# Performance work log

Hardware: AMD Instinct MI355X
Metric: run time of the kernel (lower is better)

Reference implementation:

```python
import jax, jax.numpy as jnp
import numpy as np

B, S, D, H, DK, FF, NQ = 4, 1024, 512, 64, 8, 2048, 8


def _layernorm(x, w, b, eps=1e-5):
    m = x.mean(-1, keepdims=True)
    v = ((x - m) ** 2).mean(-1, keepdims=True)
    return (x - m) / jnp.sqrt(v + eps) * w + b


def setup_inputs() -> dict:
    key = jax.random.key(0)
    ks = jax.random.split(key, 24)
    std = 0.02
    inp = {
        "x": jax.random.normal(ks[0], (B, S, D), dtype=jnp.float32),
        "Wq": jax.random.normal(ks[1], (D, D)) * std,
        "bq": jnp.zeros((D,)),
        "Wk": jax.random.normal(ks[2], (D, D)) * std,
        "bk": jnp.zeros((D,)),
        "Wv": jax.random.normal(ks[3], (D, D)) * std,
        "bv": jnp.zeros((D,)),
        "theta_attn": jax.random.normal(ks[4], (DK,)) * 0.1,  # trainable RX angles
        "gate_attn": jnp.asarray(1.0, dtype=jnp.float32),
        "Wo": jax.random.normal(ks[5], (D, D)) * std,
        "bo": jnp.zeros((D,)),
        "ln1_w": jnp.ones((D,)),
        "ln1_b": jnp.zeros((D,)),
        "W1": jax.random.normal(ks[6], (FF, NQ)) * std,
        "b1": jnp.zeros((FF,)),
        "W2": jax.random.normal(ks[7], (D, FF)) * std,
        "b2": jnp.zeros((D,)),
        "phi_ffn": jax.random.normal(ks[8], (NQ,)) * 0.1,  # trainable RY angles
        "gate_ffn": jnp.asarray(1.0, dtype=jnp.float32),
        "ln2_w": jnp.ones((D,)),
        "ln2_b": jnp.zeros((D,)),
    }
    return inp


def _attention(x, Wq, bq, Wk, bk, Wv, bv, theta, gate, Wo, bo):
    q = x @ Wq.T + bq
    k = x @ Wk.T + bk
    v = x @ Wv.T + bv
    sep = lambda t: t.reshape(B, S, H, DK).transpose(0, 2, 1, 3)  # [B,H,S,DK]
    qh, kh, vh = sep(q), sep(k), sep(v)
    scores = jnp.einsum("bhsd,bhtd->bhst", qh, kh) / np.sqrt(DK)
    probs = jax.nn.softmax(scores, axis=-1)
    classical = jnp.einsum("bhst,bhtd->bhsd", probs, vh)
    classical = classical.transpose(0, 2, 1, 3).reshape(B, S, D)
    # Quantum head: RX(x_i) then RX(theta_i) -> RX(x_i+theta_i), CNOT ring, <Z_j>.
    # Analytic expectations: <Z_0> = prod_{k=1..DK-1} cos(a_k);
    #                        <Z_j> = prod_{k=0..j}    cos(a_k)   (j >= 1).
    cos_a = jnp.cos(qh + theta)  # [B,H,S,DK]
    cp = jnp.cumprod(cos_a, axis=-1)
    z0 = jnp.prod(cos_a[..., 1:], axis=-1, keepdims=True)
    quantum = jnp.concatenate([z0, cp[..., 1:]], axis=-1)  # [B,H,S,DK]
    quantum = quantum.transpose(0, 2, 1, 3).reshape(B, S, D)
    out = gate * quantum + (1.0 - gate) * classical
    return out @ Wo.T + bo


def _ffn(x, W1, b1, W2, b2, phi, gate):
    xs = x[..., :NQ]  # encoder uses first NQ features
    # Quantum: RX(x_i) then RY(phi_i), measure <Z_i> = cos(x_i)*cos(phi_i).
    qm = jnp.cos(xs) * jnp.cos(phi)
    quantum = jax.nn.relu(qm @ W1.T + b1) @ W2.T + b2
    classical = jax.nn.relu(xs @ W1.T + b1) @ W2.T + b2
    return gate * quantum + (1.0 - gate) * classical


def reference(x, Wq, bq, Wk, bk, Wv, bv, theta_attn, gate_attn, Wo, bo,
              ln1_w, ln1_b, W1, b1, W2, b2, phi_ffn, gate_ffn, ln2_w, ln2_b):
    attn_out = _attention(x, Wq, bq, Wk, bk, Wv, bv, theta_attn, gate_attn, Wo, bo)
    x1 = _layernorm(x + attn_out, ln1_w, ln1_b)
    ffn_out = _ffn(x1, W1, b1, W2, b2, phi_ffn, gate_ffn)
    return _layernorm(x1 + ffn_out, ln2_w, ln2_b)
```

## Files before the change

### kernel.cpp

```cpp
#include <hip/hip_runtime.h>
#include <hip/hip_bf16.h>


typedef short short8 __attribute__((ext_vector_type(8)));
typedef float floatx4 __attribute__((ext_vector_type(4)));

__device__ __forceinline__ unsigned short f2bf_bits(float f) {
  __hip_bfloat16 h = __float2bfloat16(f);
  return *reinterpret_cast<unsigned short*>(&h);
}

#define GLOBAL_LOAD_LDS16(g, l)                                               \
  __builtin_amdgcn_global_load_lds(                                           \
      (const __attribute__((address_space(1))) void*)(g),                     \
      (__attribute__((address_space(3))) void*)(l), 16, 0, 0)

#define WAIT_VMCNT0()   asm volatile("s_waitcnt vmcnt(0)" ::: "memory")
#define WAIT_VMCNT16()  asm volatile("s_waitcnt vmcnt(16)" ::: "memory")
#define WAIT_LGKM0()    asm volatile("s_waitcnt lgkmcnt(0)" ::: "memory")

__global__ __launch_bounds__(64) void gemm64(
    const __hip_bfloat16* __restrict__ A,
    const __hip_bfloat16* __restrict__ W,
    const __hip_bfloat16* __restrict__ Wb,
    const float* __restrict__ bias,
    const float* __restrict__ biasb,
    float* __restrict__ Cf,
    float* __restrict__ Cfb,
    __hip_bfloat16* __restrict__ Cb,
    int M, int N, int K, int mode,
    const float* __restrict__ theta,
    const float* __restrict__ gate,
    __hip_bfloat16* __restrict__ mixout,
    const float* __restrict__ skipgate)
{
  if (skipgate != nullptr && *skipgate == 1.0f) return;
  if (blockIdx.z == 1) { W = Wb; bias = biasb; Cf = Cfb; }
  __shared__ __align__(16) __hip_bfloat16 sh[16384];
  const int lane = threadIdx.x;
  const long m0 = (long)blockIdx.x * 64;
  const long n0 = (long)blockIdx.y * 64;

  floatx4 acc[4][4];
#pragma unroll
  for (int i = 0; i < 4; ++i)
#pragma unroll
    for (int j = 0; j < 4; ++j)
      acc[i][j] = (floatx4){0.f, 0.f, 0.f, 0.f};

  const int srow = lane >> 3;
  const int schunk = lane & 7;
  const int gchunk = schunk ^ srow;
  const int frow = lane & 15;
  const int fk = lane >> 4;

  auto stage = [&](int kt, __hip_bfloat16* Ab, __hip_bfloat16* Bb) {
#pragma unroll
    for (int ib = 0; ib < 8; ++ib) {
      const int row = ib * 8 + srow;
      GLOBAL_LOAD_LDS16(A + (m0 + row) * K + kt + gchunk * 8, Ab + ib * 512);
      GLOBAL_LOAD_LDS16(W + (n0 + row) * K + kt + gchunk * 8, Bb + ib * 512);
    }
  };

  const int ntiles = K >> 6;
  stage(0, sh, sh + 4096);
  for (int t = 0; t < ntiles; ++t) {
    __hip_bfloat16* As = sh + (t & 1) * 8192;
    __hip_bfloat16* Bs = As + 4096;
    if (t + 1 < ntiles) {
      WAIT_LGKM0();
      __hip_bfloat16* An = sh + ((t + 1) & 1) * 8192;
      stage((t + 1) << 6, An, An + 4096);
      WAIT_VMCNT16();
    } else {
      WAIT_VMCNT0();
    }
    short8 af[2][4], bf[2][4];
#pragma unroll
    for (int ks = 0; ks < 2; ++ks)
#pragma unroll
      for (int i = 0; i < 4; ++i) {
        const int ar = i * 16 + frow;
        af[ks][i] = *(const short8*)(As + ar * 64 + (((ks * 4 + fk) ^ (ar & 7)) << 3));
        bf[ks][i] = *(const short8*)(Bs + ar * 64 + (((ks * 4 + fk) ^ (ar & 7)) << 3));
      }
#pragma unroll
    for (int ks = 0; ks < 2; ++ks)
#pragma unroll
      for (int i = 0; i < 4; ++i)
#pragma unroll
        for (int j = 0; j < 4; ++j)
          acc[i][j] = __builtin_amdgcn_mfma_f32_16x16x32_bf16(
              af[ks][i], bf[ks][j], acc[i][j], 0, 0, 0);
  }

  const int col_l = lane & 15;
  const int row_l = (lane >> 4) << 2;

  if (mode == 0 || (mode == 1 && *gate != 1.0f)) {
#pragma unroll
    for (int j = 0; j < 4; ++j) {
      const long col = n0 + j * 16 + col_l;
      const float bv = bias ? bias[col] : 0.0f;
#pragma unroll
      for (int i = 0; i < 4; ++i)
#pragma unroll
        for (int r = 0; r < 4; ++r)
          Cf[(m0 + i * 16 + row_l + r) * N + col] = acc[i][j][r] + bv;
    }
  }
  if (mode == 2) {
#pragma unroll
    for (int j = 0; j < 4; ++j) {
      const long col = n0 + j * 16 + col_l;
      const float bv = bias ? bias[col] : 0.0f;
#pragma unroll
      for (int i = 0; i < 4; ++i)
#pragma unroll
        for (int r = 0; r < 4; ++r)
          Cb[(m0 + i * 16 + row_l + r) * N + col] =
              __float2bfloat16(fmaxf(acc[i][j][r] + bv, 0.0f));
    }
  }
  if (mode == 1) {
    float* shf = (float*)sh;
    WAIT_LGKM0();
#pragma unroll
    for (int j = 0; j < 4; ++j) {
      const long col = n0 + j * 16 + col_l;
      const float bv = bias ? bias[col] : 0.0f;
#pragma unroll
      for (int i = 0; i < 4; ++i)
#pragma unroll
        for (int r = 0; r < 4; ++r)
          shf[(i * 16 + row_l + r) * 64 + j * 16 + col_l] = acc[i][j][r] + bv;
    }
    WAIT_LGKM0();
    float th[8];
#pragma unroll
    for (int i = 0; i < 8; ++i) th[i] = theta[i];
#pragma unroll
    for (int t = 0; t < 8; ++t) {
      const int gidx = t * 64 + lane;
      const int row = gidx >> 3;
      const int hh = gidx & 7;
      const float* src = shf + row * 64 + hh * 8;
      float c[8];
#pragma unroll
      for (int i = 0; i < 8; ++i) c[i] = __cosf(src[i] + th[i]);
      float o[8];
      float p = c[1];
#pragma unroll
      for (int i = 2; i < 8; ++i) p *= c[i];
      o[0] = p;
      float cp = c[0];
#pragma unroll
      for (int i = 1; i < 8; ++i) { cp *= c[i]; o[i] = cp; }
      union { unsigned short u16[8]; uint4 v; } pk;
#pragma unroll
      for (int i = 0; i < 8; ++i) pk.u16[i] = f2bf_bits(o[i]);
      *(uint4*)(mixout + (m0 + row) * N + n0 + hh * 8) = pk.v;
    }
  }
}

__device__ __forceinline__ void cvt_one(const float* s, __hip_bfloat16* d, int n,
                                        long tid, long stride) {
  const int n4 = n >> 2;
  for (long i = tid; i < n4; i += stride) {
    float4 v = ((const float4*)s)[i];
    ushort4 u;
    u.x = f2bf_bits(v.x); u.y = f2bf_bits(v.y);
    u.z = f2bf_bits(v.z); u.w = f2bf_bits(v.w);
    ((ushort4*)d)[i] = u;
  }
}

__global__ __launch_bounds__(256) void prep_inputs(
    const float* x, __hip_bfloat16* x_bf,
    const float* Wq, __hip_bfloat16* Wq_bf,
    const float* Wo, __hip_bfloat16* Wo_bf,
    const float* W2, __hip_bfloat16* W2_bf,
    const float* W1, __hip_bfloat16* W1_pad,
    const float* Wk, __hip_bfloat16* Wk_bf,
    const float* Wv, __hip_bfloat16* Wv_bf,
    const float* gateA)
{
  const long stride = (long)gridDim.x * blockDim.x;
  const long tid = (long)blockIdx.x * blockDim.x + threadIdx.x;
  cvt_one(x, x_bf, 4096 * 512, tid, stride);
  cvt_one(Wq, Wq_bf, 512 * 512, tid, stride);
  cvt_one(Wo, Wo_bf, 512 * 512, tid, stride);
  cvt_one(W2, W2_bf, 512 * 2048, tid, stride);
  for (long g = tid; g < 2048 * 16; g += stride) {
    const int row = g >> 4;
    const int c4 = (g & 15) << 2;
    ushort4 u = {0, 0, 0, 0};
    if (c4 < 8) {
      float4 v = *(const float4*)(W1 + row * 8 + c4);
      u.x = f2bf_bits(v.x); u.y = f2bf_bits(v.y);
      u.z = f2bf_bits(v.z); u.w = f2bf_bits(v.w);
    }
    ((ushort4*)W1_pad)[g] = u;
  }
  if (*gateA != 1.0f) {
    cvt_one(Wk, Wk_bf, 512 * 512, tid, stride);
    cvt_one(Wv, Wv_bf, 512 * 512, tid, stride);
  }
}

__global__ __launch_bounds__(256) void lnffn(
    const float* __restrict__ x, const float* __restrict__ attn,
    const float* __restrict__ w, const float* __restrict__ bias,
    float* __restrict__ x1, const float* __restrict__ phi,
    __hip_bfloat16* __restrict__ qm_pad, __hip_bfloat16* __restrict__ xs_pad,
    const float* __restrict__ gateF)
{
  const int row = blockIdx.x;
  const int tid = threadIdx.x;
  const long base = (long)row * 512;
  const int c0 = tid * 2;
  float2 av = *(const float2*)(x + base + c0);
  float2 bv = *(const float2*)(attn + base + c0);
  float s0 = av.x + bv.x, s1 = av.y + bv.y;
  float sum = s0 + s1, ssq = s0 * s0 + s1 * s1;
#pragma unroll
  for (int off = 32; off > 0; off >>= 1) {
    sum += __shfl_down(sum, off);
    ssq += __shfl_down(ssq, off);
  }
  __shared__ float red[8];
  __shared__ float qtmp[8];
  const int wv = tid >> 6, ln = tid & 63;
  if (ln == 0) { red[wv] = sum; red[4 + wv] = ssq; }
  __syncthreads();
  if (tid == 0) {
    float ts = red[0] + red[1] + red[2] + red[3];
    float tq = red[4] + red[5] + red[6] + red[7];
    float mean = ts * (1.0f / 512.0f);
    float var = tq * (1.0f / 512.0f) - mean * mean;
    red[0] = mean;
    red[1] = rsqrtf(fmaxf(var, 0.0f) + 1e-5f);
  }
  __syncthreads();
  const float mean = red[0], rstd = red[1];
  const float o0 = (s0 - mean) * rstd * w[c0] + bias[c0];
  const float o1 = (s1 - mean) * rstd * w[c0 + 1] + bias[c0 + 1];
  float2 ov; ov.x = o0; ov.y = o1;
  *(float2*)(x1 + base + c0) = ov;
  if (c0 < 8) { qtmp[c0] = o0; qtmp[c0 + 1] = o1; }
  __syncthreads();
  const float gf = *gateF;
  if (tid < 32) {
    ushort2 q = {0, 0};
    if (c0 < 8) {
      q.x = f2bf_bits(__cosf(qtmp[c0]) * __cosf(phi[c0]));
      q.y = f2bf_bits(__cosf(qtmp[c0 + 1]) * __cosf(phi[c0 + 1]));
    }
    *(ushort2*)(qm_pad + (long)row * 64 + c0) = q;
    if (gf != 1.0f) {
      ushort2 xs = {0, 0};
      if (c0 < 8) { xs.x = f2bf_bits(qtmp[c0]); xs.y = f2bf_bits(qtmp[c0 + 1]); }
      *(ushort2*)(xs_pad + (long)row * 64 + c0) = xs;
    }
  }
}

__global__ __launch_bounds__(256) void add_ln2(
    const float* __restrict__ a, const float* __restrict__ b,
    const float* __restrict__ b_alt, const float* __restrict__ gate,
    const float* __restrict__ w, const float* __restrict__ bias,
    float* __restrict__ out)
{
  const int row = blockIdx.x;
  const int tid = threadIdx.x;
  const long base = (long)row * 512;
  const int c0 = tid * 2;
  float2 av = *(const float2*)(a + base + c0);
  float2 bv = *(const float2*)(b + base + c0);
  float s0, s1;
  const float gv = *gate;
  if (gv != 1.0f) {
    float2 cv = *(const float2*)(b_alt + base + c0);
    s0 = av.x + gv * bv.x + (1.0f - gv) * cv.x;
    s1 = av.y + gv * bv.y + (1.0f - gv) * cv.y;
  } else {
    s0 = av.x + bv.x;
    s1 = av.y + bv.y;
  }
  float sum = s0 + s1, ssq = s0 * s0 + s1 * s1;
#pragma unroll
  for (int off = 32; off > 0; off >>= 1) {
    sum += __shfl_down(sum, off);
    ssq += __shfl_down(ssq, off);
  }
  __shared__ float red[8];
  const int wv = tid >> 6, ln = tid & 63;
  if (ln == 0) { red[wv] = sum; red[4 + wv] = ssq; }
  __syncthreads();
  if (tid == 0) {
    float ts = red[0] + red[1] + red[2] + red[3];
    float tq = red[4] + red[5] + red[6] + red[7];
    float mean = ts * (1.0f / 512.0f);
    float var = tq * (1.0f / 512.0f) - mean * mean;
    red[0] = mean;
    red[1] = rsqrtf(fmaxf(var, 0.0f) + 1e-5f);
  }
  __syncthreads();
  const float mean = red[0], rstd = red[1];
  float2 ov;
  ov.x = (s0 - mean) * rstd * w[c0] + bias[c0];
  ov.y = (s1 - mean) * rstd * w[c0 + 1] + bias[c0 + 1];
  *(float2*)(out + base + c0) = ov;
}

__global__ __launch_bounds__(256) void mixfix(
    __hip_bfloat16* __restrict__ mix, const float* __restrict__ cls,
    const float* __restrict__ gate, int n)
{
  const float g = *gate;
  if (g == 1.0f) return;
  const long stride = (long)gridDim.x * blockDim.x;
  for (long i = (long)blockIdx.x * blockDim.x + threadIdx.x; i < n; i += stride) {
    float q = __bfloat162float(mix[i]);
    mix[i] = __float2bfloat16(g * q + (1.0f - g) * cls[i]);
  }
}

__global__ __launch_bounds__(256) void attn_classical(
    const float* __restrict__ Q, const float* __restrict__ Kb,
    const float* __restrict__ Vb, float* __restrict__ cls,
    const float* __restrict__ skipgate)
{
  if (*skipgate == 1.0f) return;
  const int idx = blockIdx.x * blockDim.x + threadIdx.x;
  if (idx >= 4 * 64 * 1024) return;
  const int s = idx & 1023;
  const int h = (idx >> 10) & 63;
  const int b = idx >> 16;
  const long qoff = ((long)(b * 1024 + s)) * 512 + h * 8;
  float q[8];
#pragma unroll
  for (int i = 0; i < 8; ++i) q[i] = Q[qoff + i] * 0.35355339059327373f;
  float m = -INFINITY, l = 0.0f, acc[8];
#pragma unroll
  for (int i = 0; i < 8; ++i) acc[i] = 0.0f;
  for (int t = 0; t < 1024; ++t) {
    const long koff = ((long)(b * 1024 + t)) * 512 + h * 8;
    const float* kr = Kb + koff;
    const float* vr = Vb + koff;
    float sc = 0.0f;
#pragma unroll
    for (int i = 0; i < 8; ++i) sc += q[i] * kr[i];
    float nm = fmaxf(m, sc);
    float corr = __expf(m - nm);
    float p = __expf(sc - nm);
    l = l * corr + p;
#pragma unroll
    for (int i = 0; i < 8; ++i) acc[i] = acc[i] * corr + p * vr[i];
    m = nm;
  }
  const float inv = 1.0f / l;
#pragma unroll
  for (int i = 0; i < 8; ++i) cls[qoff + i] = acc[i] * inv;
}

extern "C" void kernel_launch(void* const* d_in, const int* in_sizes, int n_in,
                              void* d_out, int out_size, void* d_ws, size_t ws_size,
                              hipStream_t stream) {
  const float* x     = (const float*)d_in[0];
  const float* Wq    = (const float*)d_in[1];
  const float* bq    = (const float*)d_in[2];
  const float* Wk    = (const float*)d_in[3];
  const float* bk    = (const float*)d_in[4];
  const float* Wv    = (const float*)d_in[5];
  const float* bv    = (const float*)d_in[6];
  const float* theta = (const float*)d_in[7];
  const float* gateA = (const float*)d_in[8];
  const float* Wo    = (const float*)d_in[9];
  const float* bo    = (const float*)d_in[10];
  const float* ln1w  = (const float*)d_in[11];
  const float* ln1b  = (const float*)d_in[12];
  const float* W1    = (const float*)d_in[13];
  const float* b1    = (const float*)d_in[14];
  const float* W2    = (const float*)d_in[15];
  const float* b2    = (const float*)d_in[16];
  const float* phi   = (const float*)d_in[17];
  const float* gateF = (const float*)d_in[18];
  const float* ln2w  = (const float*)d_in[19];
  const float* ln2b  = (const float*)d_in[20];
  float* out = (float*)d_out;

  const size_t MB = 1024 * 1024;
  char* wsb = (char*)d_ws;
  __hip_bfloat16* x_bf   = (__hip_bfloat16*)(wsb + 0 * MB);
  __hip_bfloat16* Wq_bf  = (__hip_bfloat16*)(wsb + 4 * MB);
  __hip_bfloat16* Wo_bf  = (__hip_bfloat16*)(wsb + 4 * MB + 512 * 1024);
  __hip_bfloat16* W2_bf  = (__hip_bfloat16*)(wsb + 5 * MB);
  __hip_bfloat16* W1_pad = (__hip_bfloat16*)(wsb + 7 * MB);
  __hip_bfloat16* qm_pad = (__hip_bfloat16*)(wsb + 7 * MB + 512 * 1024);
  __hip_bfloat16* mix_bf = (__hip_bfloat16*)(wsb + 8 * MB);
  float*          attn   = (float*)(wsb + 12 * MB);
  float*          x1     = (float*)(wsb + 20 * MB);
  __hip_bfloat16* hq_bf  = (__hip_bfloat16*)(wsb + 28 * MB);
  float*          Fb     = (float*)(wsb + 44 * MB);
  float*          Qb     = (float*)(wsb + 52 * MB);
  __hip_bfloat16* Wk_bf  = (__hip_bfloat16*)(wsb + 60 * MB);
  __hip_bfloat16* Wv_bf  = (__hip_bfloat16*)(wsb + 60 * MB + 512 * 1024);
  float*          Kb2    = (float*)(wsb + 61 * MB);
  float*          Vb2    = (float*)(wsb + 69 * MB);
  float*          clsb   = (float*)(wsb + 77 * MB);
  __hip_bfloat16* xs_pad = (__hip_bfloat16*)(wsb + 85 * MB);
  __hip_bfloat16* hc_bf  = (__hip_bfloat16*)(wsb + 86 * MB);
  float*          Fc     = (float*)(wsb + 102 * MB);

  prep_inputs<<<1024, 256, 0, stream>>>(
      x, x_bf, Wq, Wq_bf, Wo, Wo_bf, W2, W2_bf, W1, W1_pad,
      Wk, Wk_bf, Wv, Wv_bf, gateA);
  gemm64<<<dim3(64, 8), 64, 0, stream>>>(
      x_bf, Wq_bf, nullptr, bq, nullptr, Qb, nullptr, nullptr,
      4096, 512, 512, 1, theta, gateA, mix_bf, nullptr);
  gemm64<<<dim3(64, 8, 2), 64, 0, stream>>>(
      x_bf, Wk_bf, Wv_bf, bk, bv, Kb2, Vb2, nullptr,
      4096, 512, 512, 0, nullptr, nullptr, nullptr, gateA);
  attn_classical<<<1024, 256, 0, stream>>>(Qb, Kb2, Vb2, clsb, gateA);
  mixfix<<<512, 256, 0, stream>>>(mix_bf, clsb, gateA, 4096 * 512);
  gemm64<<<dim3(64, 8), 64, 0, stream>>>(
      mix_bf, Wo_bf, nullptr, bo, nullptr, attn, nullptr, nullptr,
      4096, 512, 512, 0, nullptr, nullptr, nullptr, nullptr);
  lnffn<<<4096, 256, 0, stream>>>(x, attn, ln1w, ln1b, x1, phi,
                                  qm_pad, xs_pad, gateF);
  gemm64<<<dim3(64, 32), 64, 0, stream>>>(
      qm_pad, W1_pad, nullptr, b1, nullptr, nullptr, nullptr, hq_bf,
      4096, 2048, 64, 2, nullptr, nullptr, nullptr, nullptr);
  gemm64<<<dim3(64, 32), 64, 0, stream>>>(
      xs_pad, W1_pad, nullptr, b1, nullptr, nullptr, nullptr, hc_bf,
      4096, 2048, 64, 2, nullptr, nullptr, nullptr, gateF);
  gemm64<<<dim3(64, 8), 64, 0, stream>>>(
      hq_bf, W2_bf, nullptr, b2, nullptr, Fb, nullptr, nullptr,
      4096, 512, 2048, 0, nullptr, nullptr, nullptr, nullptr);
  gemm64<<<dim3(64, 8), 64, 0, stream>>>(
      hc_bf, W2_bf, nullptr, b2, nullptr, Fc, nullptr, nullptr,
      4096, 512, 2048, 0, nullptr, nullptr, nullptr, gateF);
  add_ln2<<<4096, 256, 0, stream>>>(x1, Fb, Fc, gateF, ln2w, ln2b, out);
}
```

Measured before the change: 175.2 us.

## Fuse W1 projection into LayerNorm kernel and merge QKV/FFN-out launches

Replaces the K=64 padded MFMA GEMM for the 8-wide W1 projection with direct FMA inside a new LayerNorm kernel that writes the ReLU hidden activations. The QKV and two FFN-output GEMMs each become a single launch that picks its operand by blockIdx.z, and the classical attention now blends straight into the mix buffer, removing the separate mixfix pass. LayerNorm kernels are rewritten to one wave per row with vectorized loads, dropping block-level syncs. This cuts launch count and the padded-GEMM and intermediate-buffer traffic, in exchange for a heavier per-thread inner product in lnffn2.

```diff
diff --git a/kernel.cpp b/kernel.cpp
--- a/kernel.cpp
+++ b/kernel.cpp
@@ -8,6 +8,11 @@
 __device__ __forceinline__ unsigned short f2bf_bits(float f) {
   __hip_bfloat16 h = __float2bfloat16(f);
   return *reinterpret_cast<unsigned short*>(&h);
+}
+__device__ __forceinline__ float bfbits2f(unsigned short u) {
+  union { unsigned int u; float f; } c;
+  c.u = (unsigned int)u << 16;
+  return c.f;
 }
 
 #define GLOBAL_LOAD_LDS16(g, l)                                               \
@@ -19,35 +24,12 @@
 #define WAIT_VMCNT16()  asm volatile("s_waitcnt vmcnt(16)" ::: "memory")
 #define WAIT_LGKM0()    asm volatile("s_waitcnt lgkmcnt(0)" ::: "memory")
 
-__global__ __launch_bounds__(64) void gemm64(
+__device__ __forceinline__ void gemm_core(
     const __hip_bfloat16* __restrict__ A,
     const __hip_bfloat16* __restrict__ W,
-    const __hip_bfloat16* __restrict__ Wb,
-    const float* __restrict__ bias,
-    const float* __restrict__ biasb,
-    float* __restrict__ Cf,
-    float* __restrict__ Cfb,
-    __hip_bfloat16* __restrict__ Cb,
-    int M, int N, int K, int mode,
-    const float* __restrict__ theta,
-    const float* __restrict__ gate,
-    __hip_bfloat16* __restrict__ mixout,
-    const float* __restrict__ skipgate)
-{
-  if (skipgate != nullptr && *skipgate == 1.0f) return;
-  if (blockIdx.z == 1) { W = Wb; bias = biasb; Cf = Cfb; }
-  __shared__ __align__(16) __hip_bfloat16 sh[16384];
-  const int lane = threadIdx.x;
-  const long m0 = (long)blockIdx.x * 64;
-  const long n0 = (long)blockIdx.y * 64;
-
-  floatx4 acc[4][4];
-#pragma unroll
-  for (int i = 0; i < 4; ++i)
-#pragma unroll
-    for (int j = 0; j < 4; ++j)
-      acc[i][j] = (floatx4){0.f, 0.f, 0.f, 0.f};
-
+    int K, long m0, long n0, int lane,
+    __hip_bfloat16* sh, floatx4 acc[4][4])
+{
   const int srow = lane >> 3;
   const int schunk = lane & 7;
   const int gchunk = schunk ^ srow;
@@ -94,42 +76,60 @@
           acc[i][j] = __builtin_amdgcn_mfma_f32_16x16x32_bf16(
               af[ks][i], bf[ks][j], acc[i][j], 0, 0, 0);
   }
+}
+
+__global__ __launch_bounds__(64) void gemm_qkv(
+    const __hip_bfloat16* __restrict__ x_bf,
+    const __hip_bfloat16* __restrict__ Wq,
+    const __hip_bfloat16* __restrict__ Wk,
+    const __hip_bfloat16* __restrict__ Wv,
+    const float* __restrict__ bq, const float* __restrict__ bk,
+    const float* __restrict__ bvv,
+    __hip_bfloat16* __restrict__ mix,
+    float* __restrict__ Qb, float* __restrict__ Kb, float* __restrict__ Vb,
+    const float* __restrict__ theta, const float* __restrict__ gateA)
+{
+  const int z = blockIdx.z;
+  const float g = *gateA;
+  if (z > 0 && g == 1.0f) return;
+  const __hip_bfloat16* W = (z == 0) ? Wq : (z == 1) ? Wk : Wv;
+  const float* bias = (z == 0) ? bq : (z == 1) ? bk : bvv;
+  float* Cf = (z == 0) ? Qb : (z == 1) ? Kb : Vb;
+
+  __shared__ __align__(16) __hip_bfloat16 sh[16384];
+  const int lane = threadIdx.x;
+  const long m0 = (long)blockIdx.x * 64;
+  const long n0 = (long)blockIdx.y * 64;
+  floatx4 acc[4][4];
+#pragma unroll
+  for (int i = 0; i < 4; ++i)
+#pragma unroll
+    for (int j = 0; j < 4; ++j) acc[i][j] = (floatx4){0.f, 0.f, 0.f, 0.f};
+
+  gemm_core(x_bf, W, 512, m0, n0, lane, sh, acc);
 
   const int col_l = lane & 15;
   const int row_l = (lane >> 4) << 2;
 
-  if (mode == 0 || (mode == 1 && *gate != 1.0f)) {
+  if (z > 0 || g != 1.0f) {
 #pragma unroll
     for (int j = 0; j < 4; ++j) {
       const long col = n0 + j * 16 + col_l;
-      const float bv = bias ? bias[col] : 0.0f;
+      const float bv = bias[col];
 #pragma unroll
       for (int i = 0; i < 4; ++i)
 #pragma unroll
         for (int r = 0; r < 4; ++r)
-          Cf[(m0 + i * 16 + row_l + r) * N + col] = acc[i][j][r] + bv;
-    }
-  }
-  if (mode == 2) {
+          Cf[(m0 + i * 16 + row_l + r) * 512 + col] = acc[i][j][r] + bv;
+    }
+  }
+  if (z == 0) {
+    float* shf = (float*)sh;
+    WAIT_LGKM0();
 #pragma unroll
     for (int j = 0; j < 4; ++j) {
       const long col = n0 + j * 16 + col_l;
-      const float bv = bias ? bias[col] : 0.0f;
-#pragma unroll
-      for (int i = 0; i < 4; ++i)
-#pragma unroll
-        for (int r = 0; r < 4; ++r)
-          Cb[(m0 + i * 16 + row_l + r) * N + col] =
-              __float2bfloat16(fmaxf(acc[i][j][r] + bv, 0.0f));
-    }
-  }
-  if (mode == 1) {
-    float* shf = (float*)sh;
-    WAIT_LGKM0();
-#pragma unroll
-    for (int j = 0; j < 4; ++j) {
-      const long col = n0 + j * 16 + col_l;
-      const float bv = bias ? bias[col] : 0.0f;
+      const float bv = bias[col];
 #pragma unroll
       for (int i = 0; i < 4; ++i)
 #pragma unroll
@@ -160,8 +160,72 @@
       union { unsigned short u16[8]; uint4 v; } pk;
 #pragma unroll
       for (int i = 0; i < 8; ++i) pk.u16[i] = f2bf_bits(o[i]);
-      *(uint4*)(mixout + (m0 + row) * N + n0 + hh * 8) = pk.v;
-    }
+      *(uint4*)(mix + (m0 + row) * 512 + n0 + hh * 8) = pk.v;
+    }
+  }
+}
+
+__global__ __launch_bounds__(64) void gemm_plain(
+    const __hip_bfloat16* __restrict__ A,
+    const __hip_bfloat16* __restrict__ W,
+    const float* __restrict__ bias, float* __restrict__ C, int N, int K)
+{
+  __shared__ __align__(16) __hip_bfloat16 sh[16384];
+  const int lane = threadIdx.x;
+  const long m0 = (long)blockIdx.x * 64;
+  const long n0 = (long)blockIdx.y * 64;
+  floatx4 acc[4][4];
+#pragma unroll
+  for (int i = 0; i < 4; ++i)
+#pragma unroll
+    for (int j = 0; j < 4; ++j) acc[i][j] = (floatx4){0.f, 0.f, 0.f, 0.f};
+  gemm_core(A, W, K, m0, n0, lane, sh, acc);
+  const int col_l = lane & 15;
+  const int row_l = (lane >> 4) << 2;
+#pragma unroll
+  for (int j = 0; j < 4; ++j) {
+    const long col = n0 + j * 16 + col_l;
+    const float bv = bias[col];
+#pragma unroll
+    for (int i = 0; i < 4; ++i)
+#pragma unroll
+      for (int r = 0; r < 4; ++r)
+        C[(m0 + i * 16 + row_l + r) * N + col] = acc[i][j][r] + bv;
+  }
+}
+
+__global__ __launch_bounds__(64) void gemm_ffnout(
+    const __hip_bfloat16* __restrict__ hq,
+    const __hip_bfloat16* __restrict__ hc,
+    const __hip_bfloat16* __restrict__ W2, const float* __restrict__ b2,
+    float* __restrict__ Fb, float* __restrict__ Fc,
+    const float* __restrict__ gateF)
+{
+  const int z = blockIdx.z;
+  if (z == 1 && *gateF == 1.0f) return;
+  const __hip_bfloat16* A = z ? hc : hq;
+  float* C = z ? Fc : Fb;
+  __shared__ __align__(16) __hip_bfloat16 sh[16384];
+  const int lane = threadIdx.x;
+  const long m0 = (long)blockIdx.x * 64;
+  const long n0 = (long)blockIdx.y * 64;
+  floatx4 acc[4][4];
+#pragma unroll
+  for (int i = 0; i < 4; ++i)
+#pragma unroll
+    for (int j = 0; j < 4; ++j) acc[i][j] = (floatx4){0.f, 0.f, 0.f, 0.f};
+  gemm_core(A, W2, 2048, m0, n0, lane, sh, acc);
+  const int col_l = lane & 15;
+  const int row_l = (lane >> 4) << 2;
+#pragma unroll
+  for (int j = 0; j < 4; ++j) {
+    const long col = n0 + j * 16 + col_l;
+    const float bv = b2[col];
+#pragma unroll
+    for (int i = 0; i < 4; ++i)
+#pragma unroll
+      for (int r = 0; r < 4; ++r)
+        C[(m0 + i * 16 + row_l + r) * 512 + col] = acc[i][j][r] + bv;
   }
 }
 
@@ -182,7 +246,7 @@
     const float* Wq, __hip_bfloat16* Wq_bf,
     const float* Wo, __hip_bfloat16* Wo_bf,
     const float* W2, __hip_bfloat16* W2_bf,
-    const float* W1, __hip_bfloat16* W1_pad,
+    const float* W1, __hip_bfloat16* W1_bf,
     const float* Wk, __hip_bfloat16* Wk_bf,
     const float* Wv, __hip_bfloat16* Wv_bf,
     const float* gateA)
@@ -193,147 +257,20 @@
   cvt_one(Wq, Wq_bf, 512 * 512, tid, stride);
   cvt_one(Wo, Wo_bf, 512 * 512, tid, stride);
   cvt_one(W2, W2_bf, 512 * 2048, tid, stride);
-  for (long g = tid; g < 2048 * 16; g += stride) {
-    const int row = g >> 4;
-    const int c4 = (g & 15) << 2;
-    ushort4 u = {0, 0, 0, 0};
-    if (c4 < 8) {
-      float4 v = *(const float4*)(W1 + row * 8 + c4);
-      u.x = f2bf_bits(v.x); u.y = f2bf_bits(v.y);
-      u.z = f2bf_bits(v.z); u.w = f2bf_bits(v.w);
-    }
-    ((ushort4*)W1_pad)[g] = u;
-  }
+  cvt_one(W1, W1_bf, 2048 * 8, tid, stride);
   if (*gateA != 1.0f) {
     cvt_one(Wk, Wk_bf, 512 * 512, tid, stride);
     cvt_one(Wv, Wv_bf, 512 * 512, tid, stride);
   }
 }
 
-__global__ __launch_bounds__(256) void lnffn(
-    const float* __restrict__ x, const float* __restrict__ attn,
-    const float* __restrict__ w, const float* __restrict__ bias,
-    float* __restrict__ x1, const float* __restrict__ phi,
-    __hip_bfloat16* __restrict__ qm_pad, __hip_bfloat16* __restrict__ xs_pad,
-    const float* __restrict__ gateF)
-{
-  const int row = blockIdx.x;
-  const int tid = threadIdx.x;
-  const long base = (long)row * 512;
-  const int c0 = tid * 2;
-  float2 av = *(const float2*)(x + base + c0);
-  float2 bv = *(const float2*)(attn + base + c0);
-  float s0 = av.x + bv.x, s1 = av.y + bv.y;
-  float sum = s0 + s1, ssq = s0 * s0 + s1 * s1;
-#pragma unroll
-  for (int off = 32; off > 0; off >>= 1) {
-    sum += __shfl_down(sum, off);
-    ssq += __shfl_down(ssq, off);
-  }
-  __shared__ float red[8];
-  __shared__ float qtmp[8];
-  const int wv = tid >> 6, ln = tid & 63;
-  if (ln == 0) { red[wv] = sum; red[4 + wv] = ssq; }
-  __syncthreads();
-  if (tid == 0) {
-    float ts = red[0] + red[1] + red[2] + red[3];
-    float tq = red[4] + red[5] + red[6] + red[7];
-    float mean = ts * (1.0f / 512.0f);
-    float var = tq * (1.0f / 512.0f) - mean * mean;
-    red[0] = mean;
-    red[1] = rsqrtf(fmaxf(var, 0.0f) + 1e-5f);
-  }
-  __syncthreads();
-  const float mean = red[0], rstd = red[1];
-  const float o0 = (s0 - mean) * rstd * w[c0] + bias[c0];
-  const float o1 = (s1 - mean) * rstd * w[c0 + 1] + bias[c0 + 1];
-  float2 ov; ov.x = o0; ov.y = o1;
-  *(float2*)(x1 + base + c0) = ov;
-  if (c0 < 8) { qtmp[c0] = o0; qtmp[c0 + 1] = o1; }
-  __syncthreads();
-  const float gf = *gateF;
-  if (tid < 32) {
-    ushort2 q = {0, 0};
-    if (c0 < 8) {
-      q.x = f2bf_bits(__cosf(qtmp[c0]) * __cosf(phi[c0]));
-      q.y = f2bf_bits(__cosf(qtmp[c0 + 1]) * __cosf(phi[c0 + 1]));
-    }
-    *(ushort2*)(qm_pad + (long)row * 64 + c0) = q;
-    if (gf != 1.0f) {
-      ushort2 xs = {0, 0};
-      if (c0 < 8) { xs.x = f2bf_bits(qtmp[c0]); xs.y = f2bf_bits(qtmp[c0 + 1]); }
-      *(ushort2*)(xs_pad + (long)row * 64 + c0) = xs;
-    }
-  }
-}
-
-__global__ __launch_bounds__(256) void add_ln2(
-    const float* __restrict__ a, const float* __restrict__ b,
-    const float* __restrict__ b_alt, const float* __restrict__ gate,
-    const float* __restrict__ w, const float* __restrict__ bias,
-    float* __restrict__ out)
-{
-  const int row = blockIdx.x;
-  const int tid = threadIdx.x;
-  const long base = (long)row * 512;
-  const int c0 = tid * 2;
-  float2 av = *(const float2*)(a + base + c0);
-  float2 bv = *(const float2*)(b + base + c0);
-  float s0, s1;
-  const float gv = *gate;
-  if (gv != 1.0f) {
-    float2 cv = *(const float2*)(b_alt + base + c0);
-    s0 = av.x + gv * bv.x + (1.0f - gv) * cv.x;
-    s1 = av.y + gv * bv.y + (1.0f - gv) * cv.y;
-  } else {
-    s0 = av.x + bv.x;
-    s1 = av.y + bv.y;
-  }
-  float sum = s0 + s1, ssq = s0 * s0 + s1 * s1;
-#pragma unroll
-  for (int off = 32; off > 0; off >>= 1) {
-    sum += __shfl_down(sum, off);
-    ssq += __shfl_down(ssq, off);
-  }
-  __shared__ float red[8];
-  const int wv = tid >> 6, ln = tid & 63;
-  if (ln == 0) { red[wv] = sum; red[4 + wv] = ssq; }
-  __syncthreads();
-  if (tid == 0) {
-    float ts = red[0] + red[1] + red[2] + red[3];
-    float tq = red[4] + red[5] + red[6] + red[7];
-    float mean = ts * (1.0f / 512.0f);
-    float var = tq * (1.0f / 512.0f) - mean * mean;
-    red[0] = mean;
-    red[1] = rsqrtf(fmaxf(var, 0.0f) + 1e-5f);
-  }
-  __syncthreads();
-  const float mean = red[0], rstd = red[1];
-  float2 ov;
-  ov.x = (s0 - mean) * rstd * w[c0] + bias[c0];
-  ov.y = (s1 - mean) * rstd * w[c0 + 1] + bias[c0 + 1];
-  *(float2*)(out + base + c0) = ov;
-}
-
-__global__ __launch_bounds__(256) void mixfix(
-    __hip_bfloat16* __restrict__ mix, const float* __restrict__ cls,
-    const float* __restrict__ gate, int n)
-{
-  const float g = *gate;
+__global__ __launch_bounds__(256) void attn_blend(
+    const float* __restrict__ Qb, const float* __restrict__ Kb,
+    const float* __restrict__ Vb, __hip_bfloat16* __restrict__ mix,
+    const float* __restrict__ gateA)
+{
+  const float g = *gateA;
   if (g == 1.0f) return;
-  const long stride = (long)gridDim.x * blockDim.x;
-  for (long i = (long)blockIdx.x * blockDim.x + threadIdx.x; i < n; i += stride) {
-    float q = __bfloat162float(mix[i]);
-    mix[i] = __float2bfloat16(g * q + (1.0f - g) * cls[i]);
-  }
-}
-
-__global__ __launch_bounds__(256) void attn_classical(
-    const float* __restrict__ Q, const float* __restrict__ Kb,
-    const float* __restrict__ Vb, float* __restrict__ cls,
-    const float* __restrict__ skipgate)
-{
-  if (*skipgate == 1.0f) return;
   const int idx = blockIdx.x * blockDim.x + threadIdx.x;
   if (idx >= 4 * 64 * 1024) return;
   const int s = idx & 1023;
@@ -342,7 +279,7 @@
   const long qoff = ((long)(b * 1024 + s)) * 512 + h * 8;
   float q[8];
 #pragma unroll
-  for (int i = 0; i < 8; ++i) q[i] = Q[qoff + i] * 0.35355339059327373f;
+  for (int i = 0; i < 8; ++i) q[i] = Qb[qoff + i] * 0.35355339059327373f;
   float m = -INFINITY, l = 0.0f, acc[8];
 #pragma unroll
   for (int i = 0; i < 8; ++i) acc[i] = 0.0f;
@@ -362,8 +299,163 @@
     m = nm;
   }
   const float inv = 1.0f / l;
-#pragma unroll
-  for (int i = 0; i < 8; ++i) cls[qoff + i] = acc[i] * inv;
+  union { unsigned short u16[8]; uint4 v; } pk;
+  pk.v = *(const uint4*)(mix + qoff);
+#pragma unroll
+  for (int i = 0; i < 8; ++i) {
+    float quant = bfbits2f(pk.u16[i]);
+    pk.u16[i] = f2bf_bits(g * quant + (1.0f - g) * acc[i] * inv);
+  }
+  *(uint4*)(mix + qoff) = pk.v;
+}
+
+__global__ __launch_bounds__(256) void lnffn2(
+    const float* __restrict__ x, const float* __restrict__ attn,
+    const float* __restrict__ lw, const float* __restrict__ lb,
+    float* __restrict__ x1, const float* __restrict__ phi,
+    const __hip_bfloat16* __restrict__ W1_bf, const float* __restrict__ b1,
+    __hip_bfloat16* __restrict__ hq, __hip_bfloat16* __restrict__ hc,
+    const float* __restrict__ gateF)
+{
+  const int tid = threadIdx.x;
+  const int wv = tid >> 6, lane = tid & 63;
+  const int row = blockIdx.x * 4 + wv;
+  const long base = (long)row * 512;
+  const int c0 = lane * 8;
+  __shared__ float qrow[4][8];
+  __shared__ float xsrow[4][8];
+
+  float4 a0 = *(const float4*)(x + base + c0);
+  float4 a1 = *(const float4*)(x + base + c0 + 4);
+  float4 b0 = *(const float4*)(attn + base + c0);
+  float4 b1v4 = *(const float4*)(attn + base + c0 + 4);
+  float s[8] = {a0.x + b0.x, a0.y + b0.y, a0.z + b0.z, a0.w + b0.w,
+                a1.x + b1v4.x, a1.y + b1v4.y, a1.z + b1v4.z, a1.w + b1v4.w};
+  float sum = 0.f, ssq = 0.f;
+#pragma unroll
+  for (int i = 0; i < 8; ++i) { sum += s[i]; ssq += s[i] * s[i]; }
+#pragma unroll
+  for (int off = 32; off > 0; off >>= 1) {
+    sum += __shfl_xor(sum, off);
+    ssq += __shfl_xor(ssq, off);
+  }
+  const float mean = sum * (1.0f / 512.0f);
+  const float var = ssq * (1.0f / 512.0f) - mean * mean;
+  const float rstd = rsqrtf(fmaxf(var, 0.0f) + 1e-5f);
+  float4 w0 = *(const float4*)(lw + c0);
+  float4 w1 = *(const float4*)(lw + c0 + 4);
+  float4 g0 = *(const float4*)(lb + c0);
+  float4 g1 = *(const float4*)(lb + c0 + 4);
+  float o[8];
+  const float wf[8] = {w0.x, w0.y, w0.z, w0.w, w1.x, w1.y, w1.z, w1.w};
+  const float gf8[8] = {g0.x, g0.y, g0.z, g0.w, g1.x, g1.y, g1.z, g1.w};
+#pragma unroll
+  for (int i = 0; i < 8; ++i) o[i] = (s[i] - mean) * rstd * wf[i] + gf8[i];
+  *(float4*)(x1 + base + c0) = (float4){o[0], o[1], o[2], o[3]};
+  *(float4*)(x1 + base + c0 + 4) = (float4){o[4], o[5], o[6], o[7]};
+  if (lane == 0) {
+#pragma unroll
+    for (int i = 0; i < 8; ++i) {
+      qrow[wv][i] = __cosf(o[i]) * __cosf(phi[i]);
+      xsrow[wv][i] = o[i];
+    }
+  }
+  __syncthreads();
+
+  float w1f[8][8];
+#pragma unroll
+  for (int j = 0; j < 8; ++j) {
+    uint4 wr = *(const uint4*)(W1_bf + (long)(tid * 8 + j) * 8);
+    const unsigned short* pu = (const unsigned short*)&wr;
+#pragma unroll
+    for (int k = 0; k < 8; ++k) w1f[j][k] = bfbits2f(pu[k]);
+  }
+  float4 bb0 = *(const float4*)(b1 + tid * 8);
+  float4 bb1 = *(const float4*)(b1 + tid * 8 + 4);
+  const float b1v[8] = {bb0.x, bb0.y, bb0.z, bb0.w, bb1.x, bb1.y, bb1.z, bb1.w};
+  const float gv = *gateF;
+#pragma unroll
+  for (int r = 0; r < 4; ++r) {
+    const long rowr = (long)blockIdx.x * 4 + r;
+    float qm[8];
+#pragma unroll
+    for (int k = 0; k < 8; ++k) qm[k] = qrow[r][k];
+    union { unsigned short u16[8]; uint4 v; } pk;
+#pragma unroll
+    for (int j = 0; j < 8; ++j) {
+      float acc = b1v[j];
+#pragma unroll
+      for (int k = 0; k < 8; ++k) acc += qm[k] * w1f[j][k];
+      pk.u16[j] = f2bf_bits(fmaxf(acc, 0.0f));
+    }
+    *(uint4*)(hq + rowr * 2048 + tid * 8) = pk.v;
+    if (gv != 1.0f) {
+      float xs[8];
+#pragma unroll
+      for (int k = 0; k < 8; ++k) xs[k] = xsrow[r][k];
+#pragma unroll
+      for (int j = 0; j < 8; ++j) {
+        float acc = b1v[j];
+#pragma unroll
+        for (int k = 0; k < 8; ++k) acc += xs[k] * w1f[j][k];
+        pk.u16[j] = f2bf_bits(fmaxf(acc, 0.0f));
+      }
+      *(uint4*)(hc + rowr * 2048 + tid * 8) = pk.v;
+    }
+  }
+}
+
+__global__ __launch_bounds__(256) void add_ln3(
+    const float* __restrict__ x1, const float* __restrict__ Fb,
+    const float* __restrict__ Fc, const float* __restrict__ gateF,
+    const float* __restrict__ lw, const float* __restrict__ lb,
+    float* __restrict__ out)
+{
+  const int tid = threadIdx.x;
+  const int wv = tid >> 6, lane = tid & 63;
+  const int row = blockIdx.x * 4 + wv;
+  const long base = (long)row * 512;
+  const int c0 = lane * 8;
+  float4 a0 = *(const float4*)(x1 + base + c0);
+  float4 a1 = *(const float4*)(x1 + base + c0 + 4);
+  float4 f0 = *(const float4*)(Fb + base + c0);
+  float4 f1 = *(const float4*)(Fb + base + c0 + 4);
+  float s[8];
+  const float gv = *gateF;
+  if (gv != 1.0f) {
+    float4 c0v = *(const float4*)(Fc + base + c0);
+    float4 c1v = *(const float4*)(Fc + base + c0 + 4);
+    const float om = 1.0f - gv;
+    s[0] = a0.x + gv * f0.x + om * c0v.x; s[1] = a0.y + gv * f0.y + om * c0v.y;
+    s[2] = a0.z + gv * f0.z + om * c0v.z; s[3] = a0.w + gv * f0.w + om * c0v.w;
+    s[4] = a1.x + gv * f1.x + om * c1v.x; s[5] = a1.y + gv * f1.y + om * c1v.y;
+    s[6] = a1.z + gv * f1.z + om * c1v.z; s[7] = a1.w + gv * f1.w + om * c1v.w;
+  } else {
+    s[0] = a0.x + f0.x; s[1] = a0.y + f0.y; s[2] = a0.z + f0.z; s[3] = a0.w + f0.w;
+    s[4] = a1.x + f1.x; s[5] = a1.y + f1.y; s[6] = a1.z + f1.z; s[7] = a1.w + f1.w;
+  }
+  float sum = 0.f, ssq = 0.f;
+#pragma unroll
+  for (int i = 0; i < 8; ++i) { sum += s[i]; ssq += s[i] * s[i]; }
+#pragma unroll
+  for (int off = 32; off > 0; off >>= 1) {
+    sum += __shfl_xor(sum, off);
+    ssq += __shfl_xor(ssq, off);
+  }
+  const float mean = sum * (1.0f / 512.0f);
+  const float var = ssq * (1.0f / 512.0f) - mean * mean;
+  const float rstd = rsqrtf(fmaxf(var, 0.0f) + 1e-5f);
+  float4 w0 = *(const float4*)(lw + c0);
+  float4 w1 = *(const float4*)(lw + c0 + 4);
+  float4 g0 = *(const float4*)(lb + c0);
+  float4 g1 = *(const float4*)(lb + c0 + 4);
+  const float wf[8] = {w0.x, w0.y, w0.z, w0.w, w1.x, w1.y, w1.z, w1.w};
+  const float gf8[8] = {g0.x, g0.y, g0.z, g0.w, g1.x, g1.y, g1.z, g1.w};
+  float o[8];
+#pragma unroll
+  for (int i = 0; i < 8; ++i) o[i] = (s[i] - mean) * rstd * wf[i] + gf8[i];
+  *(float4*)(out + base + c0) = (float4){o[0], o[1], o[2], o[3]};
+  *(float4*)(out + base + c0 + 4) = (float4){o[4], o[5], o[6], o[7]};
 }
 
 extern "C" void kernel_launch(void* const* d_in, const int* in_sizes, int n_in,
@@ -398,8 +490,7 @@
   __hip_bfloat16* Wq_bf  = (__hip_bfloat16*)(wsb + 4 * MB);
   __hip_bfloat16* Wo_bf  = (__hip_bfloat16*)(wsb + 4 * MB + 512 * 1024);
   __hip_bfloat16* W2_bf  = (__hip_bfloat16*)(wsb + 5 * MB);
-  __hip_bfloat16* W1_pad = (__hip_bfloat16*)(wsb + 7 * MB);
-  __hip_bfloat16* qm_pad = (__hip_bfloat16*)(wsb + 7 * MB + 512 * 1024);
+  __hip_bfloat16* W1_bf  = (__hip_bfloat16*)(wsb + 7 * MB);
   __hip_bfloat16* mix_bf = (__hip_bfloat16*)(wsb + 8 * MB);
   float*          attn   = (float*)(wsb + 12 * MB);
   float*          x1     = (float*)(wsb + 20 * MB);
@@ -410,38 +501,21 @@
   __hip_bfloat16* Wv_bf  = (__hip_bfloat16*)(wsb + 60 * MB + 512 * 1024);
   float*          Kb2    = (float*)(wsb + 61 * MB);
   float*          Vb2    = (float*)(wsb + 69 * MB);
-  float*          clsb   = (float*)(wsb + 77 * MB);
-  __hip_bfloat16* xs_pad = (__hip_bfloat16*)(wsb + 85 * MB);
-  __hip_bfloat16* hc_bf  = (__hip_bfloat16*)(wsb + 86 * MB);
-  float*          Fc     = (float*)(wsb + 102 * MB);
+  __hip_bfloat16* hc_bf  = (__hip_bfloat16*)(wsb + 77 * MB);
+  float*          Fc     = (float*)(wsb + 93 * MB);
 
   prep_inputs<<<1024, 256, 0, stream>>>(
-      x, x_bf, Wq, Wq_bf, Wo, Wo_bf, W2, W2_bf, W1, W1_pad,
+      x, x_bf, Wq, Wq_bf, Wo, Wo_bf, W2, W2_bf, W1, W1_bf,
       Wk, Wk_bf, Wv, Wv_bf, gateA);
-  gemm64<<<dim3(64, 8), 64, 0, stream>>>(
-      x_bf, Wq_bf, nullptr, bq, nullptr, Qb, nullptr, nullptr,
-      4096, 512, 512, 1, theta, gateA, mix_bf, nullptr);
-  gemm64<<<dim3(64, 8, 2), 64, 0, stream>>>(
-      x_bf, Wk_bf, Wv_bf, bk, bv, Kb2, Vb2, nullptr,
-      4096, 512, 512, 0, nullptr, nullptr, nullptr, gateA);
-  attn_classical<<<1024, 256, 0, stream>>>(Qb, Kb2, Vb2, clsb, gateA);
-  mixfix<<<512, 256, 0, stream>>>(mix_bf, clsb, gateA, 4096 * 512);
-  gemm64<<<dim3(64, 8), 64, 0, stream>>>(
-      mix_bf, Wo_bf, nullptr, bo, nullptr, attn, nullptr, nullptr,
-      4096, 512, 512, 0, nullptr, nullptr, nullptr, nullptr);
-  lnffn<<<4096, 256, 0, stream>>>(x, attn, ln1w, ln1b, x1, phi,
-                                  qm_pad, xs_pad, gateF);
-  gemm64<<<dim3(64, 32), 64, 0, stream>>>(
-      qm_pad, W1_pad, nullptr, b1, nullptr, nullptr, nullptr, hq_bf,
-      4096, 2048, 64, 2, nullptr, nullptr, nullptr, nullptr);
-  gemm64<<<dim3(64, 32), 64, 0, stream>>>(
-      xs_pad, W1_pad, nullptr, b1, nullptr, nullptr, nullptr, hc_bf,
-      4096, 2048, 64, 2, nullptr, nullptr, nullptr, gateF);
-  gemm64<<<dim3(64, 8), 64, 0, stream>>>(
-      hq_bf, W2_bf, nullptr, b2, nullptr, Fb, nullptr, nullptr,
-      4096, 512, 2048, 0, nullptr, nullptr, nullptr, nullptr);
-  gemm64<<<dim3(64, 8), 64, 0, stream>>>(
-      hc_bf, W2_bf, nullptr, b2, nullptr, Fc, nullptr, nullptr,
-      4096, 512, 2048, 0, nullptr, nullptr, nullptr, gateF);
-  add_ln2<<<4096, 256, 0, stream>>>(x1, Fb, Fc, gateF, ln2w, ln2b, out);
-}
+  gemm_qkv<<<dim3(64, 8, 3), 64, 0, stream>>>(
+      x_bf, Wq_bf, Wk_bf, Wv_bf, bq, bk, bv,
+      mix_bf, Qb, Kb2, Vb2, theta, gateA);
+  attn_blend<<<1024, 256, 0, stream>>>(Qb, Kb2, Vb2, mix_bf, gateA);
+  gemm_plain<<<dim3(64, 8), 64, 0, stream>>>(
+      mix_bf, Wo_bf, bo, attn, 512, 512);
+  lnffn2<<<1024, 256, 0, stream>>>(
+      x, attn, ln1w, ln1b, x1, phi, W1_bf, b1, hq_bf, hc_bf, gateF);
+  gemm_ffnout<<<dim3(64, 8, 2), 64, 0, stream>>>(
+      hq_bf, hc_bf, W2_bf, b2, Fb, Fc, gateF);
+  add_ln3<<<1024, 256, 0, stream>>>(x1, Fb, Fc, gateF, ln2w, ln2b, out);
+}
```

New measurement: 162.4 us. 7.3% less time.
